# Kernel tuning notes

Measured on AMD Instinct MI355X. Metric: run time of the kernel, lower is better.

The kernel has to match this reference:

```python
import jax, jax.numpy as jnp
import numpy as np

D_MODEL = 1024
NUM_HEAD = 16
D_HEAD = D_MODEL // NUM_HEAD
D_FFN = 4096
EPS = 1e-6


def setup_inputs() -> dict:
    key = jax.random.key(0)
    ks = jax.random.split(key, 8)
    s = 0.02
    return {
        "x": jax.random.normal(ks[0], (2, 2048, D_MODEL), dtype=jnp.float32),
        "wq": jax.random.normal(ks[1], (D_MODEL, D_MODEL), dtype=jnp.float32) * s,
        "bq": jnp.zeros((D_MODEL,), jnp.float32),
        "ln1_a": jax.random.uniform(ks[2], (D_MODEL,), dtype=jnp.float32),
        "ln1_b": jnp.zeros((D_MODEL,), jnp.float32),
        "ln2_a": jax.random.uniform(ks[3], (D_MODEL,), dtype=jnp.float32),
        "ln2_b": jnp.zeros((D_MODEL,), jnp.float32),
        "w1": jax.random.normal(ks[4], (D_FFN, D_MODEL), dtype=jnp.float32) * s,
        "b1": jnp.zeros((D_FFN,), jnp.float32),
        "w2": jax.random.normal(ks[5], (D_MODEL, D_FFN), dtype=jnp.float32) * s,
        "b2": jnp.zeros((D_MODEL,), jnp.float32),
    }


def _laynorm(x, a, b):
    # torch.std is unbiased (ddof=1); original divides by (std + eps)
    mean = jnp.mean(x, axis=-1, keepdims=True)
    std = jnp.std(x, axis=-1, keepdims=True, ddof=1)
    return a * ((x - mean) / (std + EPS)) + b


def reference(x, wq, bq, ln1_a, ln1_b, ln2_a, ln2_b, w1, b1, w2, b2):
    B, S, D = x.shape
    # NOTE: original applies Wq to Q, K, and V (Wk/Wv unused); Wo never applied.
    h = x @ wq.T + bq                      # [B,S,D]
    h = h.reshape(B, S, NUM_HEAD, D_HEAD)  # q = k = v = h
    scale = 1.0 / jnp.sqrt(jnp.float32(D_HEAD))
    scores = jnp.einsum("bqhd,bkhd->bhqk", h, h) * scale  # [B,H,S,S]
    att = jax.nn.softmax(scores, axis=-1)
    att_out = jnp.einsum("bhqk,bkhd->bqhd", att, h).reshape(B, S, D)
    # dropout is identity at inference
    x1 = _laynorm(x + att_out, ln1_a, ln1_b)
    ffn = jax.nn.relu(x1 @ w1.T + b1) @ w2.T + b2
    return _laynorm(x1 + ffn, ln2_a, ln2_b)
```

## Files before the change

### kernel.cpp

```cpp
#include <hip/hip_runtime.h>

typedef __bf16 bf16v8 __attribute__((ext_vector_type(8)));
typedef float f32x4 __attribute__((ext_vector_type(4)));

#define AS1 __attribute__((address_space(1)))
#define AS3 __attribute__((address_space(3)))

__device__ __forceinline__ void gl_lds16(const void* g, void* s) {
  __builtin_amdgcn_global_load_lds((const AS1 void*)g, (AS3 void*)s, 16, 0, 0);
}

__device__ __forceinline__ unsigned short f2b(float f) {
  union { float f; unsigned u; } v; v.f = f;
  unsigned r = v.u + 0x7fffu + ((v.u >> 16) & 1u);
  return (unsigned short)(r >> 16);
}

__device__ __forceinline__ unsigned fbits(float f) {
  union { float f; unsigned u; } v; v.f = f;
  return v.u;
}

__device__ __forceinline__ float bitsf(unsigned u) {
  union { unsigned u; float f; } v; v.u = u;
  return v.f;
}

__global__ __launch_bounds__(256) void cvt_bf16(const float* __restrict__ in,
                                                unsigned short* __restrict__ out, int n4) {
  int i = blockIdx.x * 256 + threadIdx.x;
  if (i < n4) {
    float4 v = *(const float4*)(in + (long)i * 4);
    ushort4 u = make_ushort4(f2b(v.x), f2b(v.y), f2b(v.z), f2b(v.w));
    *(ushort4*)(out + (long)i * 4) = u;
  }
}

template <int RELU, int SPLIT>
__global__ __launch_bounds__(512, 2) void gemm256p(const unsigned short* __restrict__ A,
                                                   const unsigned short* __restrict__ B,
                                                   const float* __restrict__ bias,
                                                   unsigned short* __restrict__ Cb,
                                                   int M, int N, int K, int Ks) {
  __shared__ unsigned short As[2][2][8192];
  __shared__ unsigned short Bs[2][2][8192];

  const int tid = threadIdx.x;
  const int wave = tid >> 6, lane = tid & 63;
  const int wr = wave >> 2, wc = wave & 3;
  const int g = lane >> 4, l15 = lane & 15;

  const int gx = gridDim.x;
  const int nwg = gx * gridDim.y;
  const int lin = blockIdx.y * gx + blockIdx.x;
  const int cpx = nwg >> 3;
  const int swz = (lin & 7) * cpx + (lin >> 3);
  const long m0 = (long)(swz / gx) * 256;
  const long n0 = (long)(swz % gx) * 256;
  const int kBase = blockIdx.z * Ks;

  const int srow = lane >> 2;
  const int schunk = ((lane & 3) ^ ((lane >> 3) & 3)) * 8;

  auto stA = [&](int buf, int kk, int kb) {
#pragma unroll
    for (int j = 0; j < 2; ++j) {
      const int seg = wave * 2 + j;
      gl_lds16(A + (m0 + seg * 16 + srow) * (long)K + kb + kk * 32 + schunk,
               &As[buf][kk][seg * 512]);
    }
  };
  auto stB = [&](int buf, int kk, int kb) {
#pragma unroll
    for (int j = 0; j < 2; ++j) {
      const int seg = wave * 2 + j;
      gl_lds16(B + (n0 + seg * 16 + srow) * (long)K + kb + kk * 32 + schunk,
               &Bs[buf][kk][seg * 512]);
    }
  };

  const int sel = (l15 >> 1) & 3;
  const int colA = (g ^ sel) << 3;

  f32x4 acc[8][4] = {};
  const int nt = Ks >> 6;

  stA(0, 0, kBase); stB(0, 0, kBase); stA(0, 1, kBase); stB(0, 1, kBase);
  asm volatile("s_waitcnt vmcnt(4)" ::: "memory");
  __builtin_amdgcn_s_barrier();

  int cur = 0;
  for (int t = 0; t < nt; ++t) {
    const bool pf = (t + 1 < nt);
    const int kbn = kBase + ((t + 1) << 6);
    bf16v8 af[8], b0, b1, b2, b3;

#pragma unroll
    for (int m = 0; m < 8; ++m)
      af[m] = *(const bf16v8*)&As[cur][0][(wr * 128 + m * 16 + l15) * 32 + colA];
    b0 = *(const bf16v8*)&Bs[cur][0][(wc * 64 + 0 * 16 + l15) * 32 + colA];
    b1 = *(const bf16v8*)&Bs[cur][0][(wc * 64 + 1 * 16 + l15) * 32 + colA];
    if (pf) stA(cur ^ 1, 0, kbn);
    __builtin_amdgcn_s_barrier();
    asm volatile("s_waitcnt lgkmcnt(0)" ::: "memory");
    __builtin_amdgcn_s_setprio(1);
#pragma unroll
    for (int m = 0; m < 8; ++m) {
      acc[m][0] = __builtin_amdgcn_mfma_f32_16x16x32_bf16(af[m], b0, acc[m][0], 0, 0, 0);
      acc[m][1] = __builtin_amdgcn_mfma_f32_16x16x32_bf16(af[m], b1, acc[m][1], 0, 0, 0);
    }
    __builtin_amdgcn_s_setprio(0);
    __builtin_amdgcn_s_barrier();

    b2 = *(const bf16v8*)&Bs[cur][0][(wc * 64 + 2 * 16 + l15) * 32 + colA];
    b3 = *(const bf16v8*)&Bs[cur][0][(wc * 64 + 3 * 16 + l15) * 32 + colA];
    if (pf) stB(cur ^ 1, 0, kbn);
    __builtin_amdgcn_s_barrier();
    asm volatile("s_waitcnt lgkmcnt(0)" ::: "memory");
    __builtin_amdgcn_s_setprio(1);
#pragma unroll
    for (int m = 0; m < 8; ++m) {
      acc[m][2] = __builtin_amdgcn_mfma_f32_16x16x32_bf16(af[m], b2, acc[m][2], 0, 0, 0);
      acc[m][3] = __builtin_amdgcn_mfma_f32_16x16x32_bf16(af[m], b3, acc[m][3], 0, 0, 0);
    }
    __builtin_amdgcn_s_setprio(0);
    if (pf) { asm volatile("s_waitcnt vmcnt(4)" ::: "memory"); }
    else    { asm volatile("s_waitcnt vmcnt(0)" ::: "memory"); }
    __builtin_amdgcn_s_barrier();

#pragma unroll
    for (int m = 0; m < 8; ++m)
      af[m] = *(const bf16v8*)&As[cur][1][(wr * 128 + m * 16 + l15) * 32 + colA];
    b0 = *(const bf16v8*)&Bs[cur][1][(wc * 64 + 0 * 16 + l15) * 32 + colA];
    b1 = *(const bf16v8*)&Bs[cur][1][(wc * 64 + 1 * 16 + l15) * 32 + colA];
    if (pf) stA(cur ^ 1, 1, kbn);
    __builtin_amdgcn_s_barrier();
    asm volatile("s_waitcnt lgkmcnt(0)" ::: "memory");
    __builtin_amdgcn_s_setprio(1);
#pragma unroll
    for (int m = 0; m < 8; ++m) {
      acc[m][0] = __builtin_amdgcn_mfma_f32_16x16x32_bf16(af[m], b0, acc[m][0], 0, 0, 0);
      acc[m][1] = __builtin_amdgcn_mfma_f32_16x16x32_bf16(af[m], b1, acc[m][1], 0, 0, 0);
    }
    __builtin_amdgcn_s_setprio(0);
    __builtin_amdgcn_s_barrier();

    b2 = *(const bf16v8*)&Bs[cur][1][(wc * 64 + 2 * 16 + l15) * 32 + colA];
    b3 = *(const bf16v8*)&Bs[cur][1][(wc * 64 + 3 * 16 + l15) * 32 + colA];
    if (pf) stB(cur ^ 1, 1, kbn);
    __builtin_amdgcn_s_barrier();
    asm volatile("s_waitcnt lgkmcnt(0)" ::: "memory");
    __builtin_amdgcn_s_setprio(1);
#pragma unroll
    for (int m = 0; m < 8; ++m) {
      acc[m][2] = __builtin_amdgcn_mfma_f32_16x16x32_bf16(af[m], b2, acc[m][2], 0, 0, 0);
      acc[m][3] = __builtin_amdgcn_mfma_f32_16x16x32_bf16(af[m], b3, acc[m][3], 0, 0, 0);
    }
    __builtin_amdgcn_s_setprio(0);
    if (pf) { asm volatile("s_waitcnt vmcnt(4)" ::: "memory"); }
    else    { asm volatile("s_waitcnt vmcnt(0)" ::: "memory"); }
    __builtin_amdgcn_s_barrier();

    cur ^= 1;
  }

  const long zoff = SPLIT ? (long)blockIdx.z * M * (long)N : 0;
#pragma unroll
  for (int m = 0; m < 8; ++m)
#pragma unroll
    for (int n = 0; n < 4; ++n) {
      long col = n0 + wc * 64 + n * 16 + l15;
      float bv = SPLIT ? 0.f : bias[col];
      long rowb = m0 + wr * 128 + m * 16 + g * 4;
#pragma unroll
      for (int i = 0; i < 4; ++i) {
        float v = acc[m][n][i] + bv;
        if (RELU) v = fmaxf(v, 0.f);
        Cb[zoff + (rowb + i) * (long)N + col] = f2b(v);
      }
    }
}

__global__ __launch_bounds__(256) void merge4_bias(const unsigned short* __restrict__ p,
                                                   const float* __restrict__ bias,
                                                   unsigned short* __restrict__ out) {
  const long PS = 4096L * 1024L;
  long i = ((long)blockIdx.x * 256 + threadIdx.x) * 8;
  int col = (int)(i & 1023);
  float4 b0 = *(const float4*)(bias + col);
  float4 b1 = *(const float4*)(bias + col + 4);
  float acc[8] = {b0.x, b0.y, b0.z, b0.w, b1.x, b1.y, b1.z, b1.w};
#pragma unroll
  for (int sp = 0; sp < 4; ++sp) {
    uint4 u = *(const uint4*)(p + sp * PS + i);
    unsigned r[4] = {u.x, u.y, u.z, u.w};
#pragma unroll
    for (int j = 0; j < 4; ++j) {
      acc[j * 2]     += bitsf(r[j] << 16);
      acc[j * 2 + 1] += bitsf(r[j] & 0xffff0000u);
    }
  }
  unsigned short res[8];
#pragma unroll
  for (int j = 0; j < 8; ++j) res[j] = f2b(acc[j]);
  *(uint4*)(out + i) = *(uint4*)res;
}

__global__ __launch_bounds__(256) void attn_kernel(const unsigned short* __restrict__ h,
                                                   float* __restrict__ o) {
  const int bh = blockIdx.y;
  const int b = bh >> 4, head = bh & 15;
  const int q0 = blockIdx.x * 128;
  const unsigned short* hb = h + (long)b * 2048 * 1024 + head * 64;

  __shared__ unsigned short Ks[2][64 * 64];
  __shared__ unsigned short VT[80 * 72];
  __shared__ unsigned short Ps[4][32 * 72];

  const int tid = threadIdx.x, wave = tid >> 6, lane = tid & 63;
  const int g = lane >> 4, l15 = lane & 15;
  const int vcb = wave * 16;

  for (int idx = tid; idx < 16 * 72; idx += 256)
    VT[64 * 72 + idx] = (idx < 72) ? (unsigned short)0x3F80 : (unsigned short)0;

  bf16v8 qf[2][2];
#pragma unroll
  for (int qt = 0; qt < 2; ++qt)
#pragma unroll
    for (int d = 0; d < 2; ++d)
      qf[qt][d] = *(const bf16v8*)(hb + (long)(q0 + wave * 32 + qt * 16 + l15) * 1024 + d * 32 + g * 8);

  const int krow = lane >> 3;
  const int kcol = ((lane & 7) ^ (krow & 7)) << 3;

#pragma unroll
  for (int s = 0; s < 2; ++s) {
    int seg = wave * 2 + s;
    gl_lds16(hb + (long)(seg * 8 + krow) * 1024 + kcol, &Ks[0][seg * 512]);
  }
  uint4 va0, va1;
  {
    const unsigned short* vg = hb + (long)lane * 1024 + vcb;
    va0 = *(const uint4*)vg;
    va1 = *(const uint4*)(vg + 8);
  }

  f32x4 accO[2][4] = {};
  f32x4 accL[2] = {};

  const float C1 = 0.18033688011112042f;
  const float C0 = -5.7707801635558535f;

  int cur = 0;
  for (int t = 0; t < 32; ++t) {
    __syncthreads();

    {
      unsigned short vv[16];
      *(uint4*)&vv[0] = va0;
      *(uint4*)&vv[8] = va1;
#pragma unroll
      for (int j = 0; j < 16; ++j) VT[(vcb + j) * 72 + lane] = vv[j];
    }

    const unsigned short* Kc = &Ks[cur][0];
    f32x4 sf[4][2] = {};
#pragma unroll
    for (int d = 0; d < 2; ++d) {
#pragma unroll
      for (int kt = 0; kt < 4; ++kt) {
        int r = kt * 16 + l15;
        bf16v8 kf = *(const bf16v8*)&Kc[r * 64 + ((((d << 2) + g) ^ (r & 7)) << 3)];
#pragma unroll
        for (int qt = 0; qt < 2; ++qt)
          sf[kt][qt] = __builtin_amdgcn_mfma_f32_16x16x32_bf16(kf, qf[qt][d], sf[kt][qt], 0, 0, 0);
      }
    }

    if (t < 31) {
      const int k0n = (t + 1) * 64;
#pragma unroll
      for (int s = 0; s < 2; ++s) {
        int seg = wave * 2 + s;
        gl_lds16(hb + (long)(k0n + seg * 8 + krow) * 1024 + kcol, &Ks[cur ^ 1][seg * 512]);
      }
      const unsigned short* vg = hb + (long)(k0n + lane) * 1024 + vcb;
      va0 = *(const uint4*)vg;
      va1 = *(const uint4*)(vg + 8);
    }

#pragma unroll
    for (int qt = 0; qt < 2; ++qt) {
#pragma unroll
      for (int kt = 0; kt < 4; ++kt) {
        float p0 = __builtin_amdgcn_exp2f(fmaf(sf[kt][qt][0], C1, C0));
        float p1 = __builtin_amdgcn_exp2f(fmaf(sf[kt][qt][1], C1, C0));
        float p2 = __builtin_amdgcn_exp2f(fmaf(sf[kt][qt][2], C1, C0));
        float p3 = __builtin_amdgcn_exp2f(fmaf(sf[kt][qt][3], C1, C0));
        unsigned w0 = __builtin_amdgcn_perm(fbits(p1), fbits(p0), 0x07060302u);
        unsigned w1 = __builtin_amdgcn_perm(fbits(p3), fbits(p2), 0x07060302u);
        *(uint2*)&Ps[wave][(qt * 16 + l15) * 72 + kt * 16 + g * 4] = make_uint2(w0, w1);
      }
    }

    __syncthreads();

#pragma unroll
    for (int ks = 0; ks < 2; ++ks) {
      bf16v8 pa[2];
#pragma unroll
      for (int qt = 0; qt < 2; ++qt)
        pa[qt] = *(const bf16v8*)&Ps[wave][(qt * 16 + l15) * 72 + ks * 32 + g * 8];
      bf16v8 vl = *(const bf16v8*)&VT[(64 + l15) * 72 + ks * 32 + g * 8];
#pragma unroll
      for (int dt = 0; dt < 4; ++dt) {
        bf16v8 vf = *(const bf16v8*)&VT[(dt * 16 + l15) * 72 + ks * 32 + g * 8];
#pragma unroll
        for (int qt = 0; qt < 2; ++qt)
          accO[qt][dt] = __builtin_amdgcn_mfma_f32_16x16x32_bf16(pa[qt], vf, accO[qt][dt], 0, 0, 0);
      }
#pragma unroll
      for (int qt = 0; qt < 2; ++qt)
        accL[qt] = __builtin_amdgcn_mfma_f32_16x16x32_bf16(pa[qt], vl, accL[qt], 0, 0, 0);
    }
    cur ^= 1;
  }

#pragma unroll
  for (int qt = 0; qt < 2; ++qt)
#pragma unroll
    for (int i = 0; i < 4; ++i) {
      float linv = 1.f / __shfl(accL[qt][i], lane & 48);
      long row = (long)b * 2048 + q0 + wave * 32 + qt * 16 + g * 4 + i;
#pragma unroll
      for (int dt = 0; dt < 4; ++dt)
        o[row * 1024 + head * 64 + dt * 16 + l15] = accO[qt][dt][i] * linv;
    }
}

template <int WB>
__global__ __launch_bounds__(256) void ln_add(const float* __restrict__ xa,
                                              const float* __restrict__ xb,
                                              const float* __restrict__ g,
                                              const float* __restrict__ be,
                                              float* __restrict__ of,
                                              unsigned short* __restrict__ ob) {
  const long base = (long)blockIdx.x * 1024;
  const int t = threadIdx.x;
  float4 va = *(const float4*)(xa + base + t * 4);
  float4 vb = *(const float4*)(xb + base + t * 4);
  float v0 = va.x + vb.x, v1 = va.y + vb.y, v2 = va.z + vb.z, v3 = va.w + vb.w;
  float s = v0 + v1 + v2 + v3;
  float sq = v0 * v0 + v1 * v1 + v2 * v2 + v3 * v3;
#pragma unroll
  for (int m = 1; m < 64; m <<= 1) { s += __shfl_xor(s, m); sq += __shfl_xor(sq, m); }
  __shared__ float red[8];
  const int wave = t >> 6, lane = t & 63;
  if (lane == 0) { red[wave] = s; red[4 + wave] = sq; }
  __syncthreads();
  s = red[0] + red[1] + red[2] + red[3];
  sq = red[4] + red[5] + red[6] + red[7];
  float mean = s * (1.f / 1024.f);
  float var = fmaxf(sq - s * mean, 0.f) * (1.f / 1023.f);
  float inv = 1.f / (sqrtf(var) + 1e-6f);
  float4 gg = *(const float4*)(g + t * 4);
  float4 bb = *(const float4*)(be + t * 4);
  float y0 = gg.x * ((v0 - mean) * inv) + bb.x;
  float y1 = gg.y * ((v1 - mean) * inv) + bb.y;
  float y2 = gg.z * ((v2 - mean) * inv) + bb.z;
  float y3 = gg.w * ((v3 - mean) * inv) + bb.w;
  *(float4*)(of + base + t * 4) = make_float4(y0, y1, y2, y3);
  if (WB) {
    ushort4 u = make_ushort4(f2b(y0), f2b(y1), f2b(y2), f2b(y3));
    *(ushort4*)(ob + base + t * 4) = u;
  }
}

__global__ __launch_bounds__(256) void ln_add_red4(const float* __restrict__ xa,
                                                   const unsigned short* __restrict__ zp,
                                                   const float* __restrict__ bias,
                                                   const float* __restrict__ g,
                                                   const float* __restrict__ be,
                                                   float* __restrict__ of) {
  const long base = (long)blockIdx.x * 1024;
  const int t = threadIdx.x;
  const long PS = 4096L * 1024L;
  float4 va = *(const float4*)(xa + base + t * 4);
  float4 bz = *(const float4*)(bias + t * 4);
  float v0 = va.x + bz.x, v1 = va.y + bz.y, v2 = va.z + bz.z, v3 = va.w + bz.w;
#pragma unroll
  for (int sp = 0; sp < 4; ++sp) {
    uint2 u = *(const uint2*)(zp + sp * PS + base + t * 4);
    v0 += bitsf(u.x << 16);
    v1 += bitsf(u.x & 0xffff0000u);
    v2 += bitsf(u.y << 16);
    v3 += bitsf(u.y & 0xffff0000u);
  }
  float s = v0 + v1 + v2 + v3;
  float sq = v0 * v0 + v1 * v1 + v2 * v2 + v3 * v3;
#pragma unroll
  for (int m = 1; m < 64; m <<= 1) { s += __shfl_xor(s, m); sq += __shfl_xor(sq, m); }
  __shared__ float red[8];
  const int wave = t >> 6, lane = t & 63;
  if (lane == 0) { red[wave] = s; red[4 + wave] = sq; }
  __syncthreads();
  s = red[0] + red[1] + red[2] + red[3];
  sq = red[4] + red[5] + red[6] + red[7];
  float mean = s * (1.f / 1024.f);
  float var = fmaxf(sq - s * mean, 0.f) * (1.f / 1023.f);
  float inv = 1.f / (sqrtf(var) + 1e-6f);
  float4 gg = *(const float4*)(g + t * 4);
  float4 bb = *(const float4*)(be + t * 4);
  float y0 = gg.x * ((v0 - mean) * inv) + bb.x;
  float y1 = gg.y * ((v1 - mean) * inv) + bb.y;
  float y2 = gg.z * ((v2 - mean) * inv) + bb.z;
  float y3 = gg.w * ((v3 - mean) * inv) + bb.w;
  *(float4*)(of + base + t * 4) = make_float4(y0, y1, y2, y3);
}

extern "C" void kernel_launch(void* const* d_in, const int* in_sizes, int n_in,
                              void* d_out, int out_size, void* d_ws, size_t ws_size,
                              hipStream_t stream) {
  const float* x    = (const float*)d_in[0];
  const float* wq   = (const float*)d_in[1];
  const float* bq   = (const float*)d_in[2];
  const float* ln1a = (const float*)d_in[3];
  const float* ln1b = (const float*)d_in[4];
  const float* ln2a = (const float*)d_in[5];
  const float* ln2b = (const float*)d_in[6];
  const float* w1   = (const float*)d_in[7];
  const float* b1   = (const float*)d_in[8];
  const float* w2   = (const float*)d_in[9];
  const float* b2   = (const float*)d_in[10];
  float* out = (float*)d_out;

  char* ws = (char*)d_ws;
  const size_t MB = 1024 * 1024;
  unsigned short* xb  = (unsigned short*)(ws);
  unsigned short* wqb = (unsigned short*)(ws + 8 * MB);
  unsigned short* w1b = (unsigned short*)(ws + 10 * MB);
  unsigned short* w2b = (unsigned short*)(ws + 18 * MB);
  unsigned short* qp  = (unsigned short*)(ws + 26 * MB);
  unsigned short* hb  = (unsigned short*)(ws + 58 * MB);
  float*          att = (float*)(ws + 66 * MB);
  unsigned short* yb  = (unsigned short*)(ws + 26 * MB);
  unsigned short* zp  = (unsigned short*)(ws + 58 * MB);
  float*          x1f = (float*)(ws + 90 * MB);
  unsigned short* x1b = (unsigned short*)(ws + 106 * MB);

  cvt_bf16<<<4096, 256, 0, stream>>>(x, xb, 1048576);
  cvt_bf16<<<1024, 256, 0, stream>>>(wq, wqb, 262144);
  cvt_bf16<<<4096, 256, 0, stream>>>(w1, w1b, 1048576);
  cvt_bf16<<<4096, 256, 0, stream>>>(w2, w2b, 1048576);

  gemm256p<0, 1><<<dim3(4, 16, 4), 512, 0, stream>>>(xb, wqb, nullptr, qp,
                                                     4096, 1024, 1024, 256);
  merge4_bias<<<2048, 256, 0, stream>>>(qp, bq, hb);

  attn_kernel<<<dim3(16, 32), 256, 0, stream>>>(hb, att);

  ln_add<1><<<4096, 256, 0, stream>>>(x, att, ln1a, ln1b, x1f, x1b);

  gemm256p<1, 0><<<dim3(16, 16, 1), 512, 0, stream>>>(x1b, w1b, b1, yb,
                                                      4096, 4096, 1024, 1024);

  gemm256p<0, 1><<<dim3(4, 16, 4), 512, 0, stream>>>(yb, w2b, nullptr, zp,
                                                     4096, 1024, 4096, 1024);

  ln_add_red4<<<4096, 256, 0, stream>>>(x1f, zp, b2, ln2a, ln2b, out);
}
```

Baseline: 208.8 us.

## Split attention over two KV halves and merge partials in the layernorm

The attention kernel gains a third grid dimension that splits the 2048-key range into two halves, doubling the number of workgroups. Each split writes its unnormalized fp32 output and row-sum to separate buffers. A new ln_att kernel adds the two partials, divides by the summed row-sum, then applies the residual add and layernorm. This raises parallelism and latency hiding on the attention stage, at the cost of extra fp32 partial-output writes and reads. The merge is exact because softmax uses a fixed exponent offset rather than a running max.

```diff
diff --git a/kernel.cpp b/kernel.cpp
--- a/kernel.cpp
+++ b/kernel.cpp
@@ -207,19 +207,24 @@
 }
 
 __global__ __launch_bounds__(256) void attn_kernel(const unsigned short* __restrict__ h,
-                                                   float* __restrict__ o) {
+                                                   float* __restrict__ oP,
+                                                   float* __restrict__ lP) {
   const int bh = blockIdx.y;
   const int b = bh >> 4, head = bh & 15;
   const int q0 = blockIdx.x * 128;
+  const int sp = blockIdx.z;
+  const int kvBase = sp * 1024;
   const unsigned short* hb = h + (long)b * 2048 * 1024 + head * 64;
 
-  __shared__ unsigned short Ks[2][64 * 64];
-  __shared__ unsigned short VT[80 * 72];
-  __shared__ unsigned short Ps[4][32 * 72];
+  __shared__ unsigned short smem[23168];
+  unsigned short* Ks0 = smem;
+  unsigned short* VT  = smem + 8192;
+  unsigned short* Psb = smem + 8192 + 5760;
 
   const int tid = threadIdx.x, wave = tid >> 6, lane = tid & 63;
   const int g = lane >> 4, l15 = lane & 15;
   const int vcb = wave * 16;
+  unsigned short* Psw = Psb + wave * 2304;
 
   for (int idx = tid; idx < 16 * 72; idx += 256)
     VT[64 * 72 + idx] = (idx < 72) ? (unsigned short)0x3F80 : (unsigned short)0;
@@ -237,11 +242,11 @@
 #pragma unroll
   for (int s = 0; s < 2; ++s) {
     int seg = wave * 2 + s;
-    gl_lds16(hb + (long)(seg * 8 + krow) * 1024 + kcol, &Ks[0][seg * 512]);
+    gl_lds16(hb + (long)(kvBase + seg * 8 + krow) * 1024 + kcol, Ks0 + seg * 512);
   }
   uint4 va0, va1;
   {
-    const unsigned short* vg = hb + (long)lane * 1024 + vcb;
+    const unsigned short* vg = hb + (long)(kvBase + lane) * 1024 + vcb;
     va0 = *(const uint4*)vg;
     va1 = *(const uint4*)(vg + 8);
   }
@@ -253,7 +258,7 @@
   const float C0 = -5.7707801635558535f;
 
   int cur = 0;
-  for (int t = 0; t < 32; ++t) {
+  for (int t = 0; t < 16; ++t) {
     __syncthreads();
 
     {
@@ -264,7 +269,7 @@
       for (int j = 0; j < 16; ++j) VT[(vcb + j) * 72 + lane] = vv[j];
     }
 
-    const unsigned short* Kc = &Ks[cur][0];
+    const unsigned short* Kc = Ks0 + cur * 4096;
     f32x4 sf[4][2] = {};
 #pragma unroll
     for (int d = 0; d < 2; ++d) {
@@ -278,12 +283,12 @@
       }
     }
 
-    if (t < 31) {
-      const int k0n = (t + 1) * 64;
+    if (t < 15) {
+      const int k0n = kvBase + (t + 1) * 64;
 #pragma unroll
       for (int s = 0; s < 2; ++s) {
         int seg = wave * 2 + s;
-        gl_lds16(hb + (long)(k0n + seg * 8 + krow) * 1024 + kcol, &Ks[cur ^ 1][seg * 512]);
+        gl_lds16(hb + (long)(k0n + seg * 8 + krow) * 1024 + kcol, Ks0 + (cur ^ 1) * 4096 + seg * 512);
       }
       const unsigned short* vg = hb + (long)(k0n + lane) * 1024 + vcb;
       va0 = *(const uint4*)vg;
@@ -300,7 +305,7 @@
         float p3 = __builtin_amdgcn_exp2f(fmaf(sf[kt][qt][3], C1, C0));
         unsigned w0 = __builtin_amdgcn_perm(fbits(p1), fbits(p0), 0x07060302u);
         unsigned w1 = __builtin_amdgcn_perm(fbits(p3), fbits(p2), 0x07060302u);
-        *(uint2*)&Ps[wave][(qt * 16 + l15) * 72 + kt * 16 + g * 4] = make_uint2(w0, w1);
+        *(uint2*)&Psw[(qt * 16 + l15) * 72 + kt * 16 + g * 4] = make_uint2(w0, w1);
       }
     }
 
@@ -311,7 +316,7 @@
       bf16v8 pa[2];
 #pragma unroll
       for (int qt = 0; qt < 2; ++qt)
-        pa[qt] = *(const bf16v8*)&Ps[wave][(qt * 16 + l15) * 72 + ks * 32 + g * 8];
+        pa[qt] = *(const bf16v8*)&Psw[(qt * 16 + l15) * 72 + ks * 32 + g * 8];
       bf16v8 vl = *(const bf16v8*)&VT[(64 + l15) * 72 + ks * 32 + g * 8];
 #pragma unroll
       for (int dt = 0; dt < 4; ++dt) {
@@ -327,30 +332,41 @@
     cur ^= 1;
   }
 
+  const long spo = (long)sp * 4096;
 #pragma unroll
   for (int qt = 0; qt < 2; ++qt)
 #pragma unroll
     for (int i = 0; i < 4; ++i) {
-      float linv = 1.f / __shfl(accL[qt][i], lane & 48);
       long row = (long)b * 2048 + q0 + wave * 32 + qt * 16 + g * 4 + i;
 #pragma unroll
       for (int dt = 0; dt < 4; ++dt)
-        o[row * 1024 + head * 64 + dt * 16 + l15] = accO[qt][dt][i] * linv;
-    }
-}
-
-template <int WB>
-__global__ __launch_bounds__(256) void ln_add(const float* __restrict__ xa,
-                                              const float* __restrict__ xb,
+        oP[(spo + row) * 1024 + head * 64 + dt * 16 + l15] = accO[qt][dt][i];
+      if (l15 == 0) lP[(spo + row) * 16 + head] = accL[qt][i];
+    }
+}
+
+__global__ __launch_bounds__(256) void ln_att(const float* __restrict__ x,
+                                              const float* __restrict__ a0,
+                                              const float* __restrict__ a1,
+                                              const float* __restrict__ l0,
+                                              const float* __restrict__ l1,
                                               const float* __restrict__ g,
                                               const float* __restrict__ be,
                                               float* __restrict__ of,
                                               unsigned short* __restrict__ ob) {
   const long base = (long)blockIdx.x * 1024;
   const int t = threadIdx.x;
-  float4 va = *(const float4*)(xa + base + t * 4);
-  float4 vb = *(const float4*)(xb + base + t * 4);
-  float v0 = va.x + vb.x, v1 = va.y + vb.y, v2 = va.z + vb.z, v3 = va.w + vb.w;
+  const int row = blockIdx.x;
+  const int hc = t >> 4;
+  float ls = l0[row * 16 + hc] + l1[row * 16 + hc];
+  float linv = 1.f / ls;
+  float4 vx = *(const float4*)(x + base + t * 4);
+  float4 p0 = *(const float4*)(a0 + base + t * 4);
+  float4 p1 = *(const float4*)(a1 + base + t * 4);
+  float v0 = vx.x + (p0.x + p1.x) * linv;
+  float v1 = vx.y + (p0.y + p1.y) * linv;
+  float v2 = vx.z + (p0.z + p1.z) * linv;
+  float v3 = vx.w + (p0.w + p1.w) * linv;
   float s = v0 + v1 + v2 + v3;
   float sq = v0 * v0 + v1 * v1 + v2 * v2 + v3 * v3;
 #pragma unroll
@@ -371,10 +387,8 @@
   float y2 = gg.z * ((v2 - mean) * inv) + bb.z;
   float y3 = gg.w * ((v3 - mean) * inv) + bb.w;
   *(float4*)(of + base + t * 4) = make_float4(y0, y1, y2, y3);
-  if (WB) {
-    ushort4 u = make_ushort4(f2b(y0), f2b(y1), f2b(y2), f2b(y3));
-    *(ushort4*)(ob + base + t * 4) = u;
-  }
+  ushort4 u = make_ushort4(f2b(y0), f2b(y1), f2b(y2), f2b(y3));
+  *(ushort4*)(ob + base + t * 4) = u;
 }
 
 __global__ __launch_bounds__(256) void ln_add_red4(const float* __restrict__ xa,
@@ -442,12 +456,15 @@
   unsigned short* w1b = (unsigned short*)(ws + 10 * MB);
   unsigned short* w2b = (unsigned short*)(ws + 18 * MB);
   unsigned short* qp  = (unsigned short*)(ws + 26 * MB);
+  float*          l0  = (float*)(ws + 26 * MB);
+  float*          l1  = (float*)(ws + 26 * MB + 256 * 1024);
+  unsigned short* yb  = (unsigned short*)(ws + 26 * MB);
   unsigned short* hb  = (unsigned short*)(ws + 58 * MB);
-  float*          att = (float*)(ws + 66 * MB);
-  unsigned short* yb  = (unsigned short*)(ws + 26 * MB);
+  float*          att0= (float*)(ws + 66 * MB);
+  float*          att1= (float*)(ws + 82 * MB);
   unsigned short* zp  = (unsigned short*)(ws + 58 * MB);
-  float*          x1f = (float*)(ws + 90 * MB);
-  unsigned short* x1b = (unsigned short*)(ws + 106 * MB);
+  float*          x1f = (float*)(ws + 98 * MB);
+  unsigned short* x1b = (unsigned short*)(ws + 114 * MB);
 
   cvt_bf16<<<4096, 256, 0, stream>>>(x, xb, 1048576);
   cvt_bf16<<<1024, 256, 0, stream>>>(wq, wqb, 262144);
@@ -458,9 +475,9 @@
                                                      4096, 1024, 1024, 256);
   merge4_bias<<<2048, 256, 0, stream>>>(qp, bq, hb);
 
-  attn_kernel<<<dim3(16, 32), 256, 0, stream>>>(hb, att);
-
-  ln_add<1><<<4096, 256, 0, stream>>>(x, att, ln1a, ln1b, x1f, x1b);
+  attn_kernel<<<dim3(16, 32, 2), 256, 0, stream>>>(hb, att0, l0);
+
+  ln_att<<<4096, 256, 0, stream>>>(x, att0, att1, l0, l1, ln1a, ln1b, x1f, x1b);
 
   gemm256p<1, 0><<<dim3(16, 16, 1), 512, 0, stream>>>(x1b, w1b, b1, yb,
                                                       4096, 4096, 1024, 1024);
```

New measurement: 214.9 us. +2.9%, slower.

## Keep attention probabilities in registers and double-buffer V with one barrier

Applied to the files above, without the earlier changes.

The attention loop no longer writes the softmax probabilities to shared memory and reads them back. It packs them straight into MFMA A-operand registers, with a permuted V row placement (vpos) so the register layout matches the key order. V^T is double-buffered in shared memory and the next tile is written after the PV MFMAs, which cuts the loop to one barrier per iteration. The trade-offs are more shared memory for the second V buffer, more register pressure, and reliance on the permutation being exactly right for correctness.

```diff
diff --git a/kernel.cpp b/kernel.cpp
--- a/kernel.cpp
+++ b/kernel.cpp
@@ -14,11 +14,6 @@
   union { float f; unsigned u; } v; v.f = f;
   unsigned r = v.u + 0x7fffu + ((v.u >> 16) & 1u);
   return (unsigned short)(r >> 16);
-}
-
-__device__ __forceinline__ unsigned fbits(float f) {
-  union { float f; unsigned u; } v; v.f = f;
-  return v.u;
 }
 
 __device__ __forceinline__ float bitsf(unsigned u) {
@@ -213,16 +208,19 @@
   const int q0 = blockIdx.x * 128;
   const unsigned short* hb = h + (long)b * 2048 * 1024 + head * 64;
 
-  __shared__ unsigned short Ks[2][64 * 64];
-  __shared__ unsigned short VT[80 * 72];
-  __shared__ unsigned short Ps[4][32 * 72];
+  __shared__ unsigned short smem[8192 + 2 * 5760];
+  unsigned short* Ks0 = smem;
+  unsigned short* VTb = smem + 8192;
 
   const int tid = threadIdx.x, wave = tid >> 6, lane = tid & 63;
   const int g = lane >> 4, l15 = lane & 15;
   const int vcb = wave * 16;
 
-  for (int idx = tid; idx < 16 * 72; idx += 256)
-    VT[64 * 72 + idx] = (idx < 72) ? (unsigned short)0x3F80 : (unsigned short)0;
+  for (int idx = tid; idx < 16 * 72; idx += 256) {
+    unsigned short v = (idx < 72) ? (unsigned short)0x3F80 : (unsigned short)0;
+    VTb[64 * 72 + idx] = v;
+    VTb[5760 + 64 * 72 + idx] = v;
+  }
 
   bf16v8 qf[2][2];
 #pragma unroll
@@ -234,10 +232,13 @@
   const int krow = lane >> 3;
   const int kcol = ((lane & 7) ^ (krow & 7)) << 3;
 
+  const int kl = lane;
+  const int vpos = ((kl >> 5) << 5) + (((kl & 15) >> 2) << 3) + (((kl >> 4) & 1) << 2) + (kl & 3);
+
 #pragma unroll
   for (int s = 0; s < 2; ++s) {
     int seg = wave * 2 + s;
-    gl_lds16(hb + (long)(seg * 8 + krow) * 1024 + kcol, &Ks[0][seg * 512]);
+    gl_lds16(hb + (long)(seg * 8 + krow) * 1024 + kcol, Ks0 + seg * 512);
   }
   uint4 va0, va1;
   {
@@ -245,6 +246,14 @@
     va0 = *(const uint4*)vg;
     va1 = *(const uint4*)(vg + 8);
   }
+  {
+    unsigned short vv[16];
+    *(uint4*)&vv[0] = va0;
+    *(uint4*)&vv[8] = va1;
+#pragma unroll
+    for (int j = 0; j < 16; ++j) VTb[(vcb + j) * 72 + vpos] = vv[j];
+  }
+  __syncthreads();
 
   f32x4 accO[2][4] = {};
   f32x4 accL[2] = {};
@@ -254,76 +263,75 @@
 
   int cur = 0;
   for (int t = 0; t < 32; ++t) {
-    __syncthreads();
-
-    {
-      unsigned short vv[16];
-      *(uint4*)&vv[0] = va0;
-      *(uint4*)&vv[8] = va1;
-#pragma unroll
-      for (int j = 0; j < 16; ++j) VT[(vcb + j) * 72 + lane] = vv[j];
-    }
-
-    const unsigned short* Kc = &Ks[cur][0];
-    f32x4 sf[4][2] = {};
-#pragma unroll
-    for (int d = 0; d < 2; ++d) {
-#pragma unroll
-      for (int kt = 0; kt < 4; ++kt) {
-        int r = kt * 16 + l15;
-        bf16v8 kf = *(const bf16v8*)&Kc[r * 64 + ((((d << 2) + g) ^ (r & 7)) << 3)];
-#pragma unroll
-        for (int qt = 0; qt < 2; ++qt)
-          sf[kt][qt] = __builtin_amdgcn_mfma_f32_16x16x32_bf16(kf, qf[qt][d], sf[kt][qt], 0, 0, 0);
-      }
-    }
-
     if (t < 31) {
       const int k0n = (t + 1) * 64;
 #pragma unroll
       for (int s = 0; s < 2; ++s) {
         int seg = wave * 2 + s;
-        gl_lds16(hb + (long)(k0n + seg * 8 + krow) * 1024 + kcol, &Ks[cur ^ 1][seg * 512]);
+        gl_lds16(hb + (long)(k0n + seg * 8 + krow) * 1024 + kcol, Ks0 + (cur ^ 1) * 4096 + seg * 512);
       }
       const unsigned short* vg = hb + (long)(k0n + lane) * 1024 + vcb;
       va0 = *(const uint4*)vg;
       va1 = *(const uint4*)(vg + 8);
     }
 
+    const unsigned short* Kc = Ks0 + cur * 4096;
+    f32x4 sf[4][2] = {};
+#pragma unroll
+    for (int d = 0; d < 2; ++d) {
+#pragma unroll
+      for (int kt = 0; kt < 4; ++kt) {
+        int r = kt * 16 + l15;
+        bf16v8 kf = *(const bf16v8*)&Kc[r * 64 + ((((d << 2) + g) ^ (r & 7)) << 3)];
+#pragma unroll
+        for (int qt = 0; qt < 2; ++qt)
+          sf[kt][qt] = __builtin_amdgcn_mfma_f32_16x16x32_bf16(kf, qf[qt][d], sf[kt][qt], 0, 0, 0);
+      }
+    }
+
+    bf16v8 pa[2][2];
 #pragma unroll
     for (int qt = 0; qt < 2; ++qt) {
-#pragma unroll
-      for (int kt = 0; kt < 4; ++kt) {
-        float p0 = __builtin_amdgcn_exp2f(fmaf(sf[kt][qt][0], C1, C0));
-        float p1 = __builtin_amdgcn_exp2f(fmaf(sf[kt][qt][1], C1, C0));
-        float p2 = __builtin_amdgcn_exp2f(fmaf(sf[kt][qt][2], C1, C0));
-        float p3 = __builtin_amdgcn_exp2f(fmaf(sf[kt][qt][3], C1, C0));
-        unsigned w0 = __builtin_amdgcn_perm(fbits(p1), fbits(p0), 0x07060302u);
-        unsigned w1 = __builtin_amdgcn_perm(fbits(p3), fbits(p2), 0x07060302u);
-        *(uint2*)&Ps[wave][(qt * 16 + l15) * 72 + kt * 16 + g * 4] = make_uint2(w0, w1);
+      float pe[4][4];
+#pragma unroll
+      for (int kt = 0; kt < 4; ++kt)
+#pragma unroll
+        for (int i = 0; i < 4; ++i)
+          pe[kt][i] = __builtin_amdgcn_exp2f(fmaf(sf[kt][qt][i], C1, C0));
+#pragma unroll
+      for (int i = 0; i < 4; ++i) {
+        pa[qt][0][i]     = (__bf16)pe[0][i];
+        pa[qt][0][i + 4] = (__bf16)pe[1][i];
+        pa[qt][1][i]     = (__bf16)pe[2][i];
+        pa[qt][1][i + 4] = (__bf16)pe[3][i];
       }
     }
 
+    const unsigned short* VTc = VTb + cur * 5760;
+#pragma unroll
+    for (int ks = 0; ks < 2; ++ks) {
+      bf16v8 vl = *(const bf16v8*)&VTc[(64 + l15) * 72 + ks * 32 + g * 8];
+#pragma unroll
+      for (int dt = 0; dt < 4; ++dt) {
+        bf16v8 vf = *(const bf16v8*)&VTc[(dt * 16 + l15) * 72 + ks * 32 + g * 8];
+#pragma unroll
+        for (int qt = 0; qt < 2; ++qt)
+          accO[qt][dt] = __builtin_amdgcn_mfma_f32_16x16x32_bf16(pa[qt][ks], vf, accO[qt][dt], 0, 0, 0);
+      }
+#pragma unroll
+      for (int qt = 0; qt < 2; ++qt)
+        accL[qt] = __builtin_amdgcn_mfma_f32_16x16x32_bf16(pa[qt][ks], vl, accL[qt], 0, 0, 0);
+    }
+
+    if (t < 31) {
+      unsigned short vv[16];
+      *(uint4*)&vv[0] = va0;
+      *(uint4*)&vv[8] = va1;
+      unsigned short* VTn = VTb + (cur ^ 1) * 5760;
+#pragma unroll
+      for (int j = 0; j < 16; ++j) VTn[(vcb + j) * 72 + vpos] = vv[j];
+    }
     __syncthreads();
-
-#pragma unroll
-    for (int ks = 0; ks < 2; ++ks) {
-      bf16v8 pa[2];
-#pragma unroll
-      for (int qt = 0; qt < 2; ++qt)
-        pa[qt] = *(const bf16v8*)&Ps[wave][(qt * 16 + l15) * 72 + ks * 32 + g * 8];
-      bf16v8 vl = *(const bf16v8*)&VT[(64 + l15) * 72 + ks * 32 + g * 8];
-#pragma unroll
-      for (int dt = 0; dt < 4; ++dt) {
-        bf16v8 vf = *(const bf16v8*)&VT[(dt * 16 + l15) * 72 + ks * 32 + g * 8];
-#pragma unroll
-        for (int qt = 0; qt < 2; ++qt)
-          accO[qt][dt] = __builtin_amdgcn_mfma_f32_16x16x32_bf16(pa[qt], vf, accO[qt][dt], 0, 0, 0);
-      }
-#pragma unroll
-      for (int qt = 0; qt < 2; ++qt)
-        accL[qt] = __builtin_amdgcn_mfma_f32_16x16x32_bf16(pa[qt], vl, accL[qt], 0, 0, 0);
-    }
     cur ^= 1;
   }
 
@@ -442,9 +450,9 @@
   unsigned short* w1b = (unsigned short*)(ws + 10 * MB);
   unsigned short* w2b = (unsigned short*)(ws + 18 * MB);
   unsigned short* qp  = (unsigned short*)(ws + 26 * MB);
+  unsigned short* yb  = (unsigned short*)(ws + 26 * MB);
   unsigned short* hb  = (unsigned short*)(ws + 58 * MB);
   float*          att = (float*)(ws + 66 * MB);
-  unsigned short* yb  = (unsigned short*)(ws + 26 * MB);
   unsigned short* zp  = (unsigned short*)(ws + 58 * MB);
   float*          x1f = (float*)(ws + 90 * MB);
   unsigned short* x1b = (unsigned short*)(ws + 106 * MB);
```

Measured after the change: 202.4 us. -3.1%, faster.
